# Performance work log

Measured on AMD Instinct MI355X. Metric: run time of the kernel, lower is better.

Reference implementation:

```python
import jax, jax.numpy as jnp
import numpy as np

HIDDEN = 1024
NUM_HEADS = 16
HEAD_SIZE = HIDDEN // NUM_HEADS  # 64
SQ, SK, B = 256, 1024, 8


def setup_inputs() -> dict:
    key = jax.random.key(0)
    ks = jax.random.split(key, 8)
    s = 0.02
    return {
        "x": jax.random.normal(ks[0], (SQ, B, HIDDEN), jnp.float32),
        "memory": jax.random.normal(ks[1], (SK, B, HIDDEN), jnp.float32),
        "Wq": jax.random.normal(ks[2], (HIDDEN, HIDDEN), jnp.float32) * s,
        "bq": jax.random.normal(ks[3], (HIDDEN,), jnp.float32) * s,
        "Wkv": jax.random.normal(ks[4], (2 * HIDDEN, HIDDEN), jnp.float32) * s,
        "bkv": jax.random.normal(ks[5], (2 * HIDDEN,), jnp.float32) * s,
        "Wd": jax.random.normal(ks[6], (HIDDEN, HIDDEN), jnp.float32) * s,
        "bd": jax.random.normal(ks[7], (HIDDEN,), jnp.float32) * s,
    }


def reference(x, memory, Wq, bq, Wkv, bkv, Wd, bd):
    # x: (Sq, B, E), memory: (Sk, B, E)  -- sequence-first layout
    Sq, Bb, E = x.shape
    Sk = memory.shape[0]
    H, Dh = NUM_HEADS, HEAD_SIZE

    q = x @ Wq.T + bq            # (Sq, B, E)
    kv = memory @ Wkv.T + bkv    # (Sk, B, 2E)

    # view (..., H, Dh) then composite permute (1,3,0,2):
    # NOTE: the original module's chained permutes put tensors in
    # (batch, head_size, seq, num_heads) layout, so the score matmul
    # contracts over num_heads and head_size acts as the head axis.
    q = q.reshape(Sq, Bb, H, Dh).transpose((1, 3, 0, 2))          # (B, Dh, Sq, H)
    kv = kv.reshape(Sk, Bb, H, 2 * Dh)
    k = kv[..., :Dh].transpose((1, 3, 0, 2))                       # (B, Dh, Sk, H)
    v = kv[..., Dh:].transpose((1, 3, 0, 2))                       # (B, Dh, Sk, H)

    scale = 1.0 / np.sqrt(float(Dh)).astype(np.float32)
    scores = jnp.einsum('bdqh,bdkh->bdqk', q, k) * scale           # (B, Dh, Sq, Sk)
    attn = jax.nn.softmax(scores, axis=-1)
    # attention_dropout omitted (eval mode / p=0)
    ctx = jnp.einsum('bdqk,bdkh->bdqh', attn, v)                   # (B, Dh, Sq, H)

    # transpose(1,2) -> (B, Sq, Dh, H), reshape concatenates Dh-major
    ctx = ctx.transpose((0, 2, 1, 3)).reshape(Bb, Sq, E)
    ctx = ctx.transpose((1, 0, 2))                                 # (Sq, B, E)
    out = ctx @ Wd.T + bd
    # output dropout omitted (eval mode / p=0)
    return out
```

## Files before the change

kernel.cpp:

```cpp
#include <hip/hip_runtime.h>


typedef float f32x4 __attribute__((ext_vector_type(4)));
typedef __bf16 bf16x8 __attribute__((ext_vector_type(8)));
typedef short s16x8 __attribute__((ext_vector_type(8)));
typedef unsigned int u32x2 __attribute__((ext_vector_type(2)));
typedef unsigned int u32x4 __attribute__((ext_vector_type(4)));

__device__ __forceinline__ unsigned short f2bf(float f) {
    unsigned int u = __builtin_bit_cast(unsigned int, f);
    u += 0x7fffu + ((u >> 16) & 1u);
    return (unsigned short)(u >> 16);
}
__device__ __forceinline__ unsigned cvt_pk_bf16(float lo, float hi_) {
    unsigned r;
    asm("v_cvt_pk_bf16_f32 %0, %1, %2" : "=v"(r) : "v"(lo), "v"(hi_));
    return r;
}
__device__ __forceinline__ s16x8 cvt8(float4 a, float4 b) {
    u32x4 r;
    r[0] = cvt_pk_bf16(a.x, a.y); r[1] = cvt_pk_bf16(a.z, a.w);
    r[2] = cvt_pk_bf16(b.x, b.y); r[3] = cvt_pk_bf16(b.z, b.w);
    return __builtin_bit_cast(s16x8, r);
}
__device__ __forceinline__ void gload_lds16(const unsigned short* g,
                                            unsigned short* l) {
    __builtin_amdgcn_global_load_lds(
        (const __attribute__((address_space(1))) void*)g,
        (__attribute__((address_space(3))) void*)l, 16, 0, 0);
}

__global__ void cvt_f32_bf16(const float* __restrict__ src,
                             unsigned short* __restrict__ dst) {
    int i = (blockIdx.x * 256 + threadIdx.x) * 8;
    float4 a = *reinterpret_cast<const float4*>(src + i);
    float4 b = *reinterpret_cast<const float4*>(src + i + 4);
    *reinterpret_cast<s16x8*>(dst + i) = cvt8(a, b);
}

__global__ void cvt_fused4(const float* __restrict__ x,
                           const float* __restrict__ mem,
                           const float* __restrict__ wq,
                           const float* __restrict__ wkv,
                           unsigned short* __restrict__ xb,
                           unsigned short* __restrict__ mb,
                           unsigned short* __restrict__ wqb,
                           unsigned short* __restrict__ wkvb) {
    long t = (long)blockIdx.x * 256 + threadIdx.x;
    const float* src; unsigned short* dst; long off;
    if (t < 262144)                { src = x;   dst = xb;   off = t; }
    else if (t < 262144 + 1048576) { src = mem; dst = mb;   off = t - 262144; }
    else if (t < 1441792)          { src = wq;  dst = wqb;  off = t - 1310720; }
    else                           { src = wkv; dst = wkvb; off = t - 1441792; }
    long i = off * 8;
    float4 a = *reinterpret_cast<const float4*>(src + i);
    float4 b = *reinterpret_cast<const float4*>(src + i + 4);
    *reinterpret_cast<s16x8*>(dst + i) = cvt8(a, b);
}

template <int OUT_BF16>
__global__ __launch_bounds__(256, 4)
void gemm_bt(const unsigned short* __restrict__ A,
             const unsigned short* __restrict__ Bw,
             const float* __restrict__ bias,
             void* __restrict__ Cout,
             int M, int N, int K, float scale) {
    __shared__ unsigned short U[16896];
    unsigned short(*As)[64] = (unsigned short(*)[64])U;
    unsigned short(*Bs)[64] = (unsigned short(*)[64])(U + 8192);

    const int tid = threadIdx.x;
    const int bm = blockIdx.x, bn = blockIdx.y;
    const int lane = tid & 63;
    const int w = tid >> 6;
    const int wr = w >> 1, wc = w & 1;
    const int l15 = lane & 15, lg = lane >> 4;

    f32x4 acc[4][4] = {};

    for (int k0 = 0; k0 < K; k0 += 64) {
#pragma unroll
        for (int it = 0; it < 8; ++it) {
            const int isB = it >> 2;
            int cbase = ((it & 3) << 8) + w * 64;
            int c = cbase + lane;
            int row = c >> 3, slotp = c & 7;
            int slot = slotp ^ (row & 7);
            const unsigned short* src = isB ? Bw : A;
            int grow = (isB ? bn : bm) * 128 + row;
            const unsigned short* gptr = src + (size_t)grow * K + k0 + slot * 8;
            unsigned short* lptr = (isB ? &Bs[0][0] : &As[0][0]) + cbase * 8;
            gload_lds16(gptr, lptr);
        }
        __syncthreads();

#pragma unroll
        for (int kk = 0; kk < 2; ++kk) {
            bf16x8 afr[4], bfr[4];
#pragma unroll
            for (int mi = 0; mi < 4; ++mi) {
                int row = wr * 64 + mi * 16 + l15;
                int slot = (kk * 4 + lg) ^ (row & 7);
                afr[mi] = *reinterpret_cast<const bf16x8*>(&As[row][slot * 8]);
            }
#pragma unroll
            for (int nj = 0; nj < 4; ++nj) {
                int row = wc * 64 + nj * 16 + l15;
                int slot = (kk * 4 + lg) ^ (row & 7);
                bfr[nj] = *reinterpret_cast<const bf16x8*>(&Bs[row][slot * 8]);
            }
#pragma unroll
            for (int mi = 0; mi < 4; ++mi)
#pragma unroll
                for (int nj = 0; nj < 4; ++nj)
                    acc[mi][nj] = __builtin_amdgcn_mfma_f32_16x16x32_bf16(
                        afr[mi], bfr[nj], acc[mi][nj], 0, 0, 0);
        }
        __syncthreads();
    }

    if (OUT_BF16) {
        unsigned short(*Cs)[132] = (unsigned short(*)[132])U;
#pragma unroll
        for (int nj = 0; nj < 4; ++nj) {
            int ln = wc * 64 + nj * 16 + l15;
            float bv = bias[bn * 128 + ln];
#pragma unroll
            for (int mi = 0; mi < 4; ++mi)
#pragma unroll
                for (int r = 0; r < 4; ++r) {
                    int lm = wr * 64 + mi * 16 + lg * 4 + r;
                    Cs[lm][ln] = f2bf((acc[mi][nj][r] + bv) * scale);
                }
        }
        __syncthreads();
#pragma unroll
        for (int p = 0; p < 8; ++p) {
            int c = p * 256 + tid;
            int row = c >> 4, seg = c & 15;
            s16x8 v = *reinterpret_cast<const s16x8*>(&Cs[row][seg * 8]);
            *reinterpret_cast<s16x8*>((unsigned short*)Cout +
                (size_t)(bm * 128 + row) * N + bn * 128 + seg * 8) = v;
        }
    } else {
#pragma unroll
        for (int nj = 0; nj < 4; ++nj) {
            int n = bn * 128 + wc * 64 + nj * 16 + l15;
            float bv = bias[n];
#pragma unroll
            for (int mi = 0; mi < 4; ++mi)
#pragma unroll
                for (int r = 0; r < 4; ++r) {
                    int m = bm * 128 + wr * 64 + mi * 16 + lg * 4 + r;
                    ((float*)Cout)[(size_t)m * N + n] = (acc[mi][nj][r] + bv) * scale;
                }
        }
    }
}

__global__ __launch_bounds__(256, 2)
void transpose_kv(const unsigned short* __restrict__ kvb,
                  unsigned short* __restrict__ Kp,
                  unsigned short* __restrict__ Vp) {
    __shared__ unsigned short Tl[32 * 1024];
    const int b = blockIdx.x, skc = blockIdx.y, dc = blockIdx.z;
    const int tid = threadIdx.x;
    const int sk0 = skc * 32;
#pragma unroll
    for (int it = 0; it < 16; ++it) {
        int c = it * 256 + tid;
        int r = c >> 7, w = c & 127;
        int seg = w >> 2, j = w & 3;
        int col = (seg >> 1) * 128 + (seg & 1) * 64 + dc * 32 + j * 8;
        s16x8 v = *reinterpret_cast<const s16x8*>(
            kvb + (size_t)((sk0 + r) * 8 + b) * 2048 + col);
        *reinterpret_cast<s16x8*>(&Tl[r * 1024 + seg * 32 + j * 8]) = v;
    }
    __syncthreads();
    const int dl = tid >> 3;
#pragma unroll
    for (int it = 0; it < 8; ++it) {
        int sub = it * 8 + (tid & 7);
        int r = sub >> 1, hh = sub & 1;
        s16x8 o;
#pragma unroll
        for (int e = 0; e < 8; ++e) {
            int h = hh * 8 + e;
            o[e] = Tl[r * 1024 + (h * 2) * 32 + dl];
        }
        *reinterpret_cast<s16x8*>(
            Kp + ((size_t)(b * 64 + dc * 32 + dl) * 1024 + sk0 + r) * 16 + hh * 8) = o;
    }
#pragma unroll
    for (int it = 0; it < 8; ++it) {
        int sub = it * 8 + (tid & 7);
        int h = sub >> 2, oct = sub & 3;
        s16x8 o;
#pragma unroll
        for (int e = 0; e < 8; ++e) {
            int r = oct * 8 + e;
            o[e] = Tl[r * 1024 + (h * 2 + 1) * 32 + dl];
        }
        *reinterpret_cast<s16x8*>(
            Vp + ((size_t)(b * 64 + dc * 32 + dl) * 32 + skc) * 512 + h * 32 + oct * 8) = o;
    }
}

__global__ __launch_bounds__(256, 2)
void transpose_q(const unsigned short* __restrict__ qb,
                 unsigned short* __restrict__ Qp) {
    __shared__ unsigned short Tl[32 * 512];
    const int b = blockIdx.x, sqc = blockIdx.y, dc = blockIdx.z;
    const int tid = threadIdx.x;
    const int sq0 = sqc * 32;
#pragma unroll
    for (int it = 0; it < 8; ++it) {
        int c = it * 256 + tid;
        int r = c >> 6, w = c & 63;
        int h = w >> 2, j = w & 3;
        s16x8 v = *reinterpret_cast<const s16x8*>(
            qb + (size_t)((sq0 + r) * 8 + b) * 1024 + h * 64 + dc * 32 + j * 8);
        *reinterpret_cast<s16x8*>(&Tl[r * 512 + h * 32 + j * 8]) = v;
    }
    __syncthreads();
    const int dl = tid >> 3;
#pragma unroll
    for (int it = 0; it < 8; ++it) {
        int sub = it * 8 + (tid & 7);
        int r = sub >> 1, hh = sub & 1;
        s16x8 o;
#pragma unroll
        for (int e = 0; e < 8; ++e)
            o[e] = Tl[r * 512 + (hh * 8 + e) * 32 + dl];
        *reinterpret_cast<s16x8*>(
            Qp + ((size_t)(b * 64 + dc * 32 + dl) * 256 + sq0 + r) * 16 + hh * 8) = o;
    }
}

__global__ __launch_bounds__(256, 4)
void attn_full(const unsigned short* __restrict__ Qp,
               const unsigned short* __restrict__ Kp,
               const unsigned short* __restrict__ Vp,
               unsigned short* __restrict__ ctxb) {
    __shared__ alignas(16) unsigned short KsU[64 * 16];
    __shared__ alignas(16) unsigned short VsU[2 * 512];
    __shared__ alignas(16) unsigned short Plds[4][2][16][40];

    const int bdh = blockIdx.x;
    const int bd = bdh >> 1, half = bdh & 1;
    const int b = bd >> 6, d = bd & 63;
    const int tid = threadIdx.x;
    const int w = tid >> 6, lane = tid & 63;
    const int l15 = lane & 15, lg = lane >> 4, effLg = lg & 1;

    s16x8 zero8 = {};
    const bf16x8 zfr = __builtin_bit_cast(bf16x8, zero8);

    bf16x8 qfr[2];
#pragma unroll
    for (int st = 0; st < 2; ++st) {
        int sq = half * 128 + w * 32 + st * 16 + l15;
        bf16x8 t = *reinterpret_cast<const bf16x8*>(
            Qp + ((size_t)bd * 256 + sq) * 16 + effLg * 8);
        qfr[st] = (lg < 2) ? t : zfr;
    }

    const int li = tid & 127;
    const bool isV = tid >= 128;
    const unsigned short* src = (isV ? Vp : Kp) + (size_t)bd * 16384 + li * 8;
    unsigned short* dst = (isV ? VsU : KsU) + li * 8;

    f32x4 ctx[2] = {};
    float lq[2] = {0.f, 0.f};

    s16x8 pfch = *reinterpret_cast<const s16x8*>(src);

    for (int it = 0; it < 16; ++it) {
        *reinterpret_cast<s16x8*>(dst) = pfch;
        __syncthreads();
        if (it < 15) pfch = *reinterpret_cast<const s16x8*>(src + (it + 1) * 1024);

        bf16x8 kf[4];
#pragma unroll
        for (int t4 = 0; t4 < 4; ++t4) {
            bf16x8 t = *reinterpret_cast<const bf16x8*>(
                KsU + (t4 * 16 + l15) * 16 + effLg * 8);
            kf[t4] = (lg < 2) ? t : zfr;
        }
        bf16x8 vf0 = *reinterpret_cast<const bf16x8*>(VsU + l15 * 32 + lg * 8);
        bf16x8 vf1 = *reinterpret_cast<const bf16x8*>(VsU + 512 + l15 * 32 + lg * 8);

#pragma unroll
        for (int st = 0; st < 2; ++st) {
            f32x4 z = {};
            f32x4 s0 = __builtin_amdgcn_mfma_f32_16x16x32_bf16(kf[0], qfr[st], z, 0, 0, 0);
            f32x4 s1 = __builtin_amdgcn_mfma_f32_16x16x32_bf16(kf[1], qfr[st], z, 0, 0, 0);
            f32x4 s2 = __builtin_amdgcn_mfma_f32_16x16x32_bf16(kf[2], qfr[st], z, 0, 0, 0);
            f32x4 s3 = __builtin_amdgcn_mfma_f32_16x16x32_bf16(kf[3], qfr[st], z, 0, 0, 0);

            float p0[4], p1[4], p2[4], p3[4];
#pragma unroll
            for (int r = 0; r < 4; ++r) {
                p0[r] = __expf(s0[r]); p1[r] = __expf(s1[r]);
                p2[r] = __expf(s2[r]); p3[r] = __expf(s3[r]);
            }
            float ps = ((p0[0] + p0[1]) + (p0[2] + p0[3])) +
                       ((p1[0] + p1[1]) + (p1[2] + p1[3])) +
                       ((p2[0] + p2[1]) + (p2[2] + p2[3])) +
                       ((p3[0] + p3[1]) + (p3[2] + p3[3]));
            ps += __shfl_xor(ps, 16);
            ps += __shfl_xor(ps, 32);
            lq[st] += ps;

            u32x2 wA, wB;
            wA[0] = cvt_pk_bf16(p0[0], p0[1]); wA[1] = cvt_pk_bf16(p0[2], p0[3]);
            wB[0] = cvt_pk_bf16(p1[0], p1[1]); wB[1] = cvt_pk_bf16(p1[2], p1[3]);
            *reinterpret_cast<u32x2*>(&Plds[w][0][l15][lg * 4]) = wA;
            *reinterpret_cast<u32x2*>(&Plds[w][0][l15][16 + lg * 4]) = wB;
            u32x2 wC, wD;
            wC[0] = cvt_pk_bf16(p2[0], p2[1]); wC[1] = cvt_pk_bf16(p2[2], p2[3]);
            wD[0] = cvt_pk_bf16(p3[0], p3[1]); wD[1] = cvt_pk_bf16(p3[2], p3[3]);
            *reinterpret_cast<u32x2*>(&Plds[w][1][l15][lg * 4]) = wC;
            *reinterpret_cast<u32x2*>(&Plds[w][1][l15][16 + lg * 4]) = wD;

            bf16x8 pfr0 = *reinterpret_cast<const bf16x8*>(&Plds[w][0][l15][lg * 8]);
            ctx[st] = __builtin_amdgcn_mfma_f32_16x16x32_bf16(pfr0, vf0, ctx[st], 0, 0, 0);
            bf16x8 pfr1 = *reinterpret_cast<const bf16x8*>(&Plds[w][1][l15][lg * 8]);
            ctx[st] = __builtin_amdgcn_mfma_f32_16x16x32_bf16(pfr1, vf1, ctx[st], 0, 0, 0);
        }
        __syncthreads();
    }

#pragma unroll
    for (int st = 0; st < 2; ++st) {
        float invown = 1.f / lq[st];
#pragma unroll
        for (int r = 0; r < 4; ++r) {
            float inv = __shfl(invown, lg * 4 + r);
            int sq = half * 128 + w * 32 + st * 16 + lg * 4 + r;
            ctxb[(size_t)(sq * 8 + b) * 1024 + d * 16 + l15] =
                f2bf(ctx[st][r] * inv);
        }
    }
}

extern "C" void kernel_launch(void* const* d_in, const int* in_sizes, int n_in,
                              void* d_out, int out_size, void* d_ws, size_t ws_size,
                              hipStream_t stream) {
    const float* x   = (const float*)d_in[0];
    const float* mem = (const float*)d_in[1];
    const float* Wq  = (const float*)d_in[2];
    const float* bq  = (const float*)d_in[3];
    const float* Wkv = (const float*)d_in[4];
    const float* bkv = (const float*)d_in[5];
    const float* Wd  = (const float*)d_in[6];
    const float* bd  = (const float*)d_in[7];
    float* out = (float*)d_out;

    const size_t M = 1024 * 1024;
    unsigned short* ws    = (unsigned short*)d_ws;
    unsigned short* qbuf  = ws;
    unsigned short* kvbuf = ws + 2 * M;
    unsigned short* Kp    = ws + 18 * M;
    unsigned short* Vp    = ws + 26 * M;
    unsigned short* xb    = ws + 18 * M;
    unsigned short* mb    = ws + 20 * M;
    unsigned short* wqb   = ws + 28 * M;
    unsigned short* wkvb  = ws + 29 * M;
    unsigned short* ctxb  = ws + 2 * M;
    unsigned short* Qp    = ws + 4 * M;
    unsigned short* wdb   = ws + 6 * M;

    cvt_fused4<<<6656, 256, 0, stream>>>(x, mem, Wq, Wkv, xb, mb, wqb, wkvb);

    gemm_bt<1><<<dim3(2048 / 128, 1024 / 128), 256, 0, stream>>>(
        xb, wqb, bq, qbuf, 2048, 1024, 1024, 0.125f);
    gemm_bt<1><<<dim3(8192 / 128, 2048 / 128), 256, 0, stream>>>(
        mb, wkvb, bkv, kvbuf, 8192, 2048, 1024, 1.0f);

    transpose_kv<<<dim3(8, 32, 2), 256, 0, stream>>>(kvbuf, Kp, Vp);
    transpose_q<<<dim3(8, 8, 2), 256, 0, stream>>>(qbuf, Qp);

    cvt_f32_bf16<<<512, 256, 0, stream>>>(Wd, wdb);

    attn_full<<<1024, 256, 0, stream>>>(Qp, Kp, Vp, ctxb);

    gemm_bt<0><<<dim3(2048 / 128, 1024 / 128), 256, 0, stream>>>(
        ctxb, wdb, bd, out, 2048, 1024, 1024, 1.0f);
}
```

Baseline: 147.2 us.

## Add 256x256-tile bf16 GEMM with interleaved prefetch for KV projection

Replaces the 128x128-tile GEMM for the memory-to-KV projection with a dedicated 512-thread kernel that uses 256x256 output tiles. Each wave computes a 128x64 region. Global-to-LDS loads for the next K step are issued in quarters between MFMA phases, with barrier and setprio scheduling. The output goes through an LDS staging buffer so stores are coalesced. Larger tiles raise arithmetic intensity and cut global traffic, at the cost of more registers and LDS, fewer blocks (256), and possible occupancy limits.

After: 150.8 us. 1.02x slower.

```diff
diff --git a/kernel.cpp b/kernel.cpp
--- a/kernel.cpp
+++ b/kernel.cpp
@@ -158,6 +158,121 @@
     }
 }
 
+__global__ __launch_bounds__(512, 2)
+void gemm256(const unsigned short* __restrict__ A,
+             const unsigned short* __restrict__ Bw,
+             const float* __restrict__ bias,
+             unsigned short* __restrict__ Cout) {
+    constexpr int K = 1024, N = 2048;
+    __shared__ unsigned short LDSU[2][2][16384];
+
+    const int tid = threadIdx.x;
+    const int bm = blockIdx.x, bn = blockIdx.y;
+    const int lane = tid & 63;
+    const int w = tid >> 6;
+    const int wm = w >> 2, wn = w & 3;
+    const int l15 = lane & 15, lg = lane >> 4;
+    const int strow = tid >> 3, stslotp = tid & 7;
+
+    f32x4 acc[8][4] = {};
+
+    auto stage_chunk = [&](int buf, int c, int kt) {
+        const int mat = c >> 2, quarter = c & 3;
+        int row = quarter * 64 + strow;
+        int slot = stslotp ^ (row & 7);
+        const unsigned short* src = mat ? Bw : A;
+        int grow = (mat ? bn : bm) * 256 + row;
+        const unsigned short* g = src + (size_t)grow * K + kt * 64 + slot * 8;
+        unsigned short* l = &LDSU[buf][mat][quarter * 4096 + tid * 8];
+        gload_lds16(g, l);
+    };
+
+#pragma unroll
+    for (int c = 0; c < 8; ++c) stage_chunk(0, c, 0);
+    asm volatile("s_waitcnt vmcnt(0)" ::: "memory");
+    __builtin_amdgcn_s_barrier();
+
+    for (int kt = 0; kt < 16; ++kt) {
+        const int cur = kt & 1;
+        const unsigned short* As = &LDSU[cur][0][0];
+        const unsigned short* Bs = &LDSU[cur][1][0];
+        const bool pf = (kt < 15);
+#pragma unroll
+        for (int q = 0; q < 4; ++q) {
+            const int qm = q >> 1, qn = q & 1;
+            bf16x8 afr[4][2], bfr[2][2];
+#pragma unroll
+            for (int i = 0; i < 4; ++i) {
+                int row = wm * 128 + (qm * 4 + i) * 16 + l15;
+#pragma unroll
+                for (int kk = 0; kk < 2; ++kk) {
+                    int slot = (kk * 4 + lg) ^ (row & 7);
+                    afr[i][kk] = *reinterpret_cast<const bf16x8*>(
+                        As + row * 64 + slot * 8);
+                }
+            }
+#pragma unroll
+            for (int j = 0; j < 2; ++j) {
+                int row = wn * 64 + (qn * 2 + j) * 16 + l15;
+#pragma unroll
+                for (int kk = 0; kk < 2; ++kk) {
+                    int slot = (kk * 4 + lg) ^ (row & 7);
+                    bfr[j][kk] = *reinterpret_cast<const bf16x8*>(
+                        Bs + row * 64 + slot * 8);
+                }
+            }
+            if (pf) {
+                stage_chunk(cur ^ 1, q * 2, kt + 1);
+                stage_chunk(cur ^ 1, q * 2 + 1, kt + 1);
+            }
+            __builtin_amdgcn_s_barrier();
+            __builtin_amdgcn_s_setprio(1);
+#pragma unroll
+            for (int i = 0; i < 4; ++i)
+#pragma unroll
+                for (int j = 0; j < 2; ++j)
+#pragma unroll
+                    for (int kk = 0; kk < 2; ++kk)
+                        acc[qm * 4 + i][qn * 2 + j] =
+                            __builtin_amdgcn_mfma_f32_16x16x32_bf16(
+                                afr[i][kk], bfr[j][kk],
+                                acc[qm * 4 + i][qn * 2 + j], 0, 0, 0);
+            __builtin_amdgcn_s_setprio(0);
+            __builtin_amdgcn_s_barrier();
+        }
+        asm volatile("s_waitcnt vmcnt(0)" ::: "memory");
+        __builtin_amdgcn_s_barrier();
+    }
+
+    unsigned short(*Cs)[260] = (unsigned short(*)[260])&LDSU[0][0][0];
+    __syncthreads();
+#pragma unroll
+    for (int pass = 0; pass < 2; ++pass) {
+        if (wm == pass) {
+#pragma unroll
+            for (int j = 0; j < 4; ++j) {
+                int lc = wn * 64 + j * 16 + l15;
+                float bv = bias[bn * 256 + lc];
+#pragma unroll
+                for (int i = 0; i < 8; ++i)
+#pragma unroll
+                    for (int r = 0; r < 4; ++r)
+                        Cs[i * 16 + lg * 4 + r][lc] = f2bf(acc[i][j][r] + bv);
+            }
+        }
+        __syncthreads();
+#pragma unroll
+        for (int p = 0; p < 8; ++p) {
+            int c = p * 512 + tid;
+            int row = c >> 5, seg = c & 31;
+            s16x8 v = *reinterpret_cast<const s16x8*>(&Cs[row][seg * 8]);
+            *reinterpret_cast<s16x8*>(Cout +
+                (size_t)(bm * 256 + pass * 128 + row) * N + bn * 256 + seg * 8) = v;
+        }
+        __syncthreads();
+    }
+}
+
 __global__ __launch_bounds__(256, 2)
 void transpose_kv(const unsigned short* __restrict__ kvb,
                   unsigned short* __restrict__ Kp,
@@ -375,12 +490,12 @@
 
     gemm_bt<1><<<dim3(2048 / 128, 1024 / 128), 256, 0, stream>>>(
         xb, wqb, bq, qbuf, 2048, 1024, 1024, 0.125f);
-    gemm_bt<1><<<dim3(8192 / 128, 2048 / 128), 256, 0, stream>>>(
-        mb, wkvb, bkv, kvbuf, 8192, 2048, 1024, 1.0f);
+
+    gemm256<<<dim3(8192 / 256, 2048 / 256), 512, 0, stream>>>(
+        mb, wkvb, bkv, kvbuf);
 
     transpose_kv<<<dim3(8, 32, 2), 256, 0, stream>>>(kvbuf, Kp, Vp);
     transpose_q<<<dim3(8, 8, 2), 256, 0, stream>>>(qbuf, Qp);
-
     cvt_f32_bf16<<<512, 256, 0, stream>>>(Wd, wdb);
 
     attn_full<<<1024, 256, 0, stream>>>(Qp, Kp, Vp, ctxb);
```
